# Kernel tuning notes

Measured on AMD Instinct MI355X. Metric: run time of the kernel, lower is better.

Reference implementation:

```python
import jax, jax.numpy as jnp
import numpy as np

B, S, D, U, A = 8, 2048, 1024, 1024, 4  # batch, seq, input_dim, units, n_activations


def setup_inputs() -> dict:
    key = jax.random.key(0)
    ks = jax.random.split(key, 6)
    scale_w = (6.0 / (D + U)) ** 0.5  # glorot_uniform
    scale_wf = (6.0 / (U + A)) ** 0.5
    scale_wa = (6.0 / (D + A)) ** 0.5
    return {
        "x": jax.random.normal(ks[0], (B, S, D), dtype=jnp.float32),
        "w": jax.random.uniform(ks[1], (D, U), jnp.float32, -scale_w, scale_w),
        "b": jnp.zeros((U,), jnp.float32),
        "wf": jax.random.uniform(ks[2], (U, A), jnp.float32, -scale_wf, scale_wf),
        "bf": jnp.zeros((U, A), jnp.float32),
        "w_att": jax.random.uniform(ks[3], (D, A), jnp.float32, -scale_wa, scale_wa),
        "b_att": jnp.zeros((A,), jnp.float32),
    }


def reference(x, w, b, wf, bf, w_att, b_att):
    # weighted_sum: [B,S,U]
    ws = jnp.einsum('bsd,du->bsu', x, w) + b
    # broadcast per-activation affine: [B,S,U,A]
    wa = ws[..., None] * wf + bf
    acts = [
        jax.nn.relu(wa[..., 0]),
        jax.nn.sigmoid(wa[..., 1]),
        jnp.tanh(wa[..., 2]),
        jax.nn.gelu(wa[..., 3], approximate=False),  # tf.nn.gelu default is exact
    ]
    result_activations = jnp.stack(acts, axis=-1)  # [B,S,U,A]
    # attention over activations: [B,S,A]
    attn = jax.nn.softmax(jnp.einsum('bsd,da->bsa', x, w_att) + b_att, axis=-1)
    # weighted reduce over activation axis -> [B,S,U]
    out = jnp.einsum('bsua,bsa->bsu', result_activations, attn)
    return out
```

## Files before the change

### kernel.cpp

```cpp
#include <hip/hip_runtime.h>
#include <hip/hip_bf16.h>
#include <cstdint>

#define B_ 8
#define S_ 2048
#define D_ 1024
#define U_ 1024
#define M_ (B_ * S_)

typedef __bf16 bf16x8 __attribute__((ext_vector_type(8)));
typedef float  f32x4  __attribute__((ext_vector_type(4)));

__device__ __forceinline__ uint16_t f2bf(float f) {
  uint32_t u = __builtin_bit_cast(uint32_t, f);
  u += 0x7fffu + ((u >> 16) & 1u);
  return (uint16_t)(u >> 16);
}

__device__ __forceinline__ void async_copy16(const void* g, void* l) {
  typedef const __attribute__((address_space(1))) uint8_t* gp_t;
  typedef __attribute__((address_space(3))) uint8_t* lp_t;
  __builtin_amdgcn_global_load_lds((gp_t)(uintptr_t)g,
                                   (lp_t)(uint32_t)(uintptr_t)l, 16, 0, 0);
}

__global__ __launch_bounds__(256) void k_conv_w(const float* __restrict__ w,
                                                uint16_t* __restrict__ wt) {
  __shared__ float tile[32][33];
  const int t = threadIdx.x;
  const int tx = t & 31, ty = t >> 5;
  const int c0 = blockIdx.x * 32;
  const int r0 = blockIdx.y * 32;
#pragma unroll
  for (int i = 0; i < 4; i++) {
    int r = ty + i * 8;
    tile[r][tx] = w[(size_t)(r0 + r) * U_ + c0 + tx];
  }
  __syncthreads();
#pragma unroll
  for (int i = 0; i < 4; i++) {
    int r = ty + i * 8;
    wt[(size_t)(c0 + r) * D_ + r0 + tx] = f2bf(tile[tx][r]);
  }
}

__global__ __launch_bounds__(256) void k_attn_convx(
    const float* __restrict__ x, const float* __restrict__ w_att,
    const float* __restrict__ b_att, uint16_t* __restrict__ x_bf,
    float* __restrict__ attn) {
  const int row = blockIdx.x;
  const int t = threadIdx.x;
  const float4 xv = reinterpret_cast<const float4*>(x + (size_t)row * D_)[t];
  float xe0 = xv.x, xe1 = xv.y, xe2 = xv.z, xe3 = xv.w;

  const float4* wa4 = reinterpret_cast<const float4*>(w_att);
  float p0 = 0.f, p1 = 0.f, p2 = 0.f, p3 = 0.f;
  float xs[4] = {xe0, xe1, xe2, xe3};
#pragma unroll
  for (int e = 0; e < 4; e++) {
    float4 wv = wa4[t * 4 + e];
    p0 = fmaf(xs[e], wv.x, p0);
    p1 = fmaf(xs[e], wv.y, p1);
    p2 = fmaf(xs[e], wv.z, p2);
    p3 = fmaf(xs[e], wv.w, p3);
  }

  ushort4 hb;
  hb.x = f2bf(xe0); hb.y = f2bf(xe1); hb.z = f2bf(xe2); hb.w = f2bf(xe3);
  reinterpret_cast<ushort4*>(x_bf + (size_t)row * D_)[t] = hb;

#pragma unroll
  for (int off = 32; off > 0; off >>= 1) {
    p0 += __shfl_down(p0, off);
    p1 += __shfl_down(p1, off);
    p2 += __shfl_down(p2, off);
    p3 += __shfl_down(p3, off);
  }
  __shared__ float red[4][4];
  const int lane = t & 63, wid = t >> 6;
  if (lane == 0) { red[wid][0] = p0; red[wid][1] = p1; red[wid][2] = p2; red[wid][3] = p3; }
  __syncthreads();
  if (t == 0) {
    float l0 = red[0][0] + red[1][0] + red[2][0] + red[3][0] + b_att[0];
    float l1 = red[0][1] + red[1][1] + red[2][1] + red[3][1] + b_att[1];
    float l2 = red[0][2] + red[1][2] + red[2][2] + red[3][2] + b_att[2];
    float l3 = red[0][3] + red[1][3] + red[2][3] + red[3][3] + b_att[3];
    float mx = fmaxf(fmaxf(l0, l1), fmaxf(l2, l3));
    float e0 = __expf(l0 - mx), e1 = __expf(l1 - mx);
    float e2 = __expf(l2 - mx), e3 = __expf(l3 - mx);
    float inv = 1.f / (e0 + e1 + e2 + e3);
    reinterpret_cast<float4*>(attn)[row] = make_float4(e0 * inv, e1 * inv, e2 * inv, e3 * inv);
  }
}

#define BM 128
#define BN 128
#define BK 64

__global__ __launch_bounds__(256) void k_gemm_ep(
    const uint16_t* __restrict__ xbf, const uint16_t* __restrict__ wt,
    const float* __restrict__ bias, const float* __restrict__ wf,
    const float* __restrict__ bfb, const float* __restrict__ attn,
    float* __restrict__ out) {
  __shared__ uint16_t As[BM * BK];
  __shared__ uint16_t Bs[BN * BK];

  const int t = threadIdx.x;
  const int wave = t >> 6, lane = t & 63;
  const int l16 = lane & 15, quad = lane >> 4;
  const int wm = wave >> 1, wn = wave & 1;
  const int m0 = blockIdx.y * BM;
  const int n0 = blockIdx.x * BN;

  const uint16_t* aBase = xbf + (size_t)m0 * D_;
  const uint16_t* bBase = wt + (size_t)n0 * D_;

  f32x4 acc[4][4] = {};

  for (int k0 = 0; k0 < D_; k0 += BK) {
#pragma unroll
    for (int it = 0; it < 4; it++) {
      int c = t + it * 256;
      int r = c >> 3;
      int cs = c & 7;
      int gc = cs ^ (r & 7);
      async_copy16(aBase + (size_t)r * D_ + k0 + gc * 8, (uint8_t*)As + c * 16);
      async_copy16(bBase + (size_t)r * D_ + k0 + gc * 8, (uint8_t*)Bs + c * 16);
    }
    __syncthreads();

#pragma unroll
    for (int ks = 0; ks < 2; ks++) {
      const int kcb = ks * 4;
      bf16x8 af[4], bfr[4];
#pragma unroll
      for (int i = 0; i < 4; i++) {
        int r = wm * 64 + i * 16 + l16;
        int cs = (kcb + quad) ^ (r & 7);
        af[i] = *reinterpret_cast<const bf16x8*>(&As[r * BK + cs * 8]);
      }
#pragma unroll
      for (int j = 0; j < 4; j++) {
        int n = wn * 64 + j * 16 + l16;
        int cs = (kcb + quad) ^ (n & 7);
        bfr[j] = *reinterpret_cast<const bf16x8*>(&Bs[n * BK + cs * 8]);
      }
#pragma unroll
      for (int i = 0; i < 4; i++)
#pragma unroll
        for (int j = 0; j < 4; j++)
          acc[i][j] = __builtin_amdgcn_mfma_f32_16x16x32_bf16(af[i], bfr[j], acc[i][j], 0, 0, 0);
    }
    __syncthreads();
  }

  float bu[4];
  float4 wf4[4], bf4[4];
#pragma unroll
  for (int j = 0; j < 4; j++) {
    int u = n0 + wn * 64 + j * 16 + l16;
    bu[j] = bias[u];
    wf4[j] = reinterpret_cast<const float4*>(wf)[u];
    bf4[j] = reinterpret_cast<const float4*>(bfb)[u];
  }
#pragma unroll
  for (int i = 0; i < 4; i++) {
#pragma unroll
    for (int r = 0; r < 4; r++) {
      int mg = m0 + wm * 64 + i * 16 + quad * 4 + r;
      float4 at = reinterpret_cast<const float4*>(attn)[mg];
      float* orow = out + (size_t)mg * U_;
#pragma unroll
      for (int j = 0; j < 4; j++) {
        int u = n0 + wn * 64 + j * 16 + l16;
        float wsv = acc[i][j][r] + bu[j];
        float wa0 = fmaf(wsv, wf4[j].x, bf4[j].x);
        float wa1 = fmaf(wsv, wf4[j].y, bf4[j].y);
        float wa2 = fmaf(wsv, wf4[j].z, bf4[j].z);
        float wa3 = fmaf(wsv, wf4[j].w, bf4[j].w);
        float a_relu = fmaxf(wa0, 0.f);
        float a_sig = 1.f / (1.f + __expf(-wa1));
        float ax = fabsf(wa2);
        float et = __expf(-2.f * ax);
        float a_tanh = copysignf((1.f - et) / (1.f + et), wa2);
        float a_gelu = 0.5f * wa3 * (1.f + erff(wa3 * 0.70710678118654752f));
        orow[u] = at.x * a_relu + at.y * a_sig + at.z * a_tanh + at.w * a_gelu;
      }
    }
  }
}

extern "C" void kernel_launch(void* const* d_in, const int* in_sizes, int n_in,
                              void* d_out, int out_size, void* d_ws, size_t ws_size,
                              hipStream_t stream) {
  const float* x     = (const float*)d_in[0];
  const float* w     = (const float*)d_in[1];
  const float* b     = (const float*)d_in[2];
  const float* wf    = (const float*)d_in[3];
  const float* bfb   = (const float*)d_in[4];
  const float* w_att = (const float*)d_in[5];
  const float* b_att = (const float*)d_in[6];
  float* out = (float*)d_out;

  char* ws = (char*)d_ws;
  uint16_t* x_bf = (uint16_t*)ws;
  uint16_t* w_t  = (uint16_t*)(ws + ((size_t)32 << 20));
  float*    attn = (float*)(ws + ((size_t)34 << 20));

  k_conv_w<<<dim3(U_ / 32, D_ / 32), 256, 0, stream>>>(w, w_t);
  k_attn_convx<<<dim3(M_), 256, 0, stream>>>(x, w_att, b_att, x_bf, attn);
  k_gemm_ep<<<dim3(U_ / BN, M_ / BM), 256, 0, stream>>>(x_bf, w_t, b, wf, bfb, attn, out);
}
```

Measured before the change: 197.6 us.

## Fuse prep kernels and use fast approximate activations in GEMM epilogue

Merges the weight-transpose and x-conversion/attention kernels into one launch, with one wave per row and xor-shuffle reduction, removing the cross-wave LDS reduction and one launch. Replaces exact sigmoid, tanh and erf-GELU in the epilogue with hardware exp2/rcp intrinsics and a tanh-form GELU approximation to cut transcendental cost. Adds an occupancy hint to the GEMM launch bounds. The GELU approximation changes numerics compared with exact erf and may affect tolerance.

```diff
diff --git a/kernel.cpp b/kernel.cpp
--- a/kernel.cpp
+++ b/kernel.cpp
@@ -24,72 +24,73 @@
                                    (lp_t)(uint32_t)(uintptr_t)l, 16, 0, 0);
 }
 
-__global__ __launch_bounds__(256) void k_conv_w(const float* __restrict__ w,
-                                                uint16_t* __restrict__ wt) {
+__global__ __launch_bounds__(256) void k_prep(
+    const float* __restrict__ x, const float* __restrict__ w_att,
+    const float* __restrict__ b_att, const float* __restrict__ w,
+    uint16_t* __restrict__ x_bf, float* __restrict__ attn,
+    uint16_t* __restrict__ wt) {
   __shared__ float tile[32][33];
-  const int t = threadIdx.x;
-  const int tx = t & 31, ty = t >> 5;
-  const int c0 = blockIdx.x * 32;
-  const int r0 = blockIdx.y * 32;
-#pragma unroll
-  for (int i = 0; i < 4; i++) {
-    int r = ty + i * 8;
-    tile[r][tx] = w[(size_t)(r0 + r) * U_ + c0 + tx];
-  }
-  __syncthreads();
-#pragma unroll
-  for (int i = 0; i < 4; i++) {
-    int r = ty + i * 8;
-    wt[(size_t)(c0 + r) * D_ + r0 + tx] = f2bf(tile[tx][r]);
-  }
-}
-
-__global__ __launch_bounds__(256) void k_attn_convx(
-    const float* __restrict__ x, const float* __restrict__ w_att,
-    const float* __restrict__ b_att, uint16_t* __restrict__ x_bf,
-    float* __restrict__ attn) {
-  const int row = blockIdx.x;
-  const int t = threadIdx.x;
-  const float4 xv = reinterpret_cast<const float4*>(x + (size_t)row * D_)[t];
-  float xe0 = xv.x, xe1 = xv.y, xe2 = xv.z, xe3 = xv.w;
-
-  const float4* wa4 = reinterpret_cast<const float4*>(w_att);
-  float p0 = 0.f, p1 = 0.f, p2 = 0.f, p3 = 0.f;
-  float xs[4] = {xe0, xe1, xe2, xe3};
-#pragma unroll
-  for (int e = 0; e < 4; e++) {
-    float4 wv = wa4[t * 4 + e];
-    p0 = fmaf(xs[e], wv.x, p0);
-    p1 = fmaf(xs[e], wv.y, p1);
-    p2 = fmaf(xs[e], wv.z, p2);
-    p3 = fmaf(xs[e], wv.w, p3);
-  }
-
-  ushort4 hb;
-  hb.x = f2bf(xe0); hb.y = f2bf(xe1); hb.z = f2bf(xe2); hb.w = f2bf(xe3);
-  reinterpret_cast<ushort4*>(x_bf + (size_t)row * D_)[t] = hb;
-
-#pragma unroll
-  for (int off = 32; off > 0; off >>= 1) {
-    p0 += __shfl_down(p0, off);
-    p1 += __shfl_down(p1, off);
-    p2 += __shfl_down(p2, off);
-    p3 += __shfl_down(p3, off);
-  }
-  __shared__ float red[4][4];
-  const int lane = t & 63, wid = t >> 6;
-  if (lane == 0) { red[wid][0] = p0; red[wid][1] = p1; red[wid][2] = p2; red[wid][3] = p3; }
-  __syncthreads();
-  if (t == 0) {
-    float l0 = red[0][0] + red[1][0] + red[2][0] + red[3][0] + b_att[0];
-    float l1 = red[0][1] + red[1][1] + red[2][1] + red[3][1] + b_att[1];
-    float l2 = red[0][2] + red[1][2] + red[2][2] + red[3][2] + b_att[2];
-    float l3 = red[0][3] + red[1][3] + red[2][3] + red[3][3] + b_att[3];
-    float mx = fmaxf(fmaxf(l0, l1), fmaxf(l2, l3));
-    float e0 = __expf(l0 - mx), e1 = __expf(l1 - mx);
-    float e2 = __expf(l2 - mx), e3 = __expf(l3 - mx);
-    float inv = 1.f / (e0 + e1 + e2 + e3);
-    reinterpret_cast<float4*>(attn)[row] = make_float4(e0 * inv, e1 * inv, e2 * inv, e3 * inv);
+  const int bid = blockIdx.x;
+  if (bid < M_ / 4) {
+    const int wave = threadIdx.x >> 6, lane = threadIdx.x & 63;
+    const int row = bid * 4 + wave;
+    const float4* xr = reinterpret_cast<const float4*>(x + (size_t)row * D_);
+    const float4* wa4 = reinterpret_cast<const float4*>(w_att);
+    float4 v[4];
+#pragma unroll
+    for (int i = 0; i < 4; i++) v[i] = xr[lane + 64 * i];
+    float4 p = {0.f, 0.f, 0.f, 0.f};
+#pragma unroll
+    for (int i = 0; i < 4; i++) {
+      const int base = 4 * (lane + 64 * i);
+      const float xe[4] = {v[i].x, v[i].y, v[i].z, v[i].w};
+#pragma unroll
+      for (int c = 0; c < 4; c++) {
+        float4 wv = wa4[base + c];
+        p.x = fmaf(xe[c], wv.x, p.x);
+        p.y = fmaf(xe[c], wv.y, p.y);
+        p.z = fmaf(xe[c], wv.z, p.z);
+        p.w = fmaf(xe[c], wv.w, p.w);
+      }
+      ushort4 hb;
+      hb.x = f2bf(v[i].x); hb.y = f2bf(v[i].y);
+      hb.z = f2bf(v[i].z); hb.w = f2bf(v[i].w);
+      reinterpret_cast<ushort4*>(x_bf + (size_t)row * D_)[lane + 64 * i] = hb;
+    }
+#pragma unroll
+    for (int off = 32; off > 0; off >>= 1) {
+      p.x += __shfl_xor(p.x, off);
+      p.y += __shfl_xor(p.y, off);
+      p.z += __shfl_xor(p.z, off);
+      p.w += __shfl_xor(p.w, off);
+    }
+    if (lane == 0) {
+      float l0 = p.x + b_att[0], l1 = p.y + b_att[1];
+      float l2 = p.z + b_att[2], l3 = p.w + b_att[3];
+      float mx = fmaxf(fmaxf(l0, l1), fmaxf(l2, l3));
+      float e0 = __expf(l0 - mx), e1 = __expf(l1 - mx);
+      float e2 = __expf(l2 - mx), e3 = __expf(l3 - mx);
+      float inv = __builtin_amdgcn_rcpf(e0 + e1 + e2 + e3);
+      reinterpret_cast<float4*>(attn)[row] =
+          make_float4(e0 * inv, e1 * inv, e2 * inv, e3 * inv);
+    }
+  } else {
+    const int wid = bid - M_ / 4;
+    const int t = threadIdx.x;
+    const int tx = t & 31, ty = t >> 5;
+    const int c0 = (wid & 31) * 32;
+    const int r0 = (wid >> 5) * 32;
+#pragma unroll
+    for (int i = 0; i < 4; i++) {
+      int r = ty + i * 8;
+      tile[r][tx] = w[(size_t)(r0 + r) * U_ + c0 + tx];
+    }
+    __syncthreads();
+#pragma unroll
+    for (int i = 0; i < 4; i++) {
+      int r = ty + i * 8;
+      wt[(size_t)(c0 + r) * D_ + r0 + tx] = f2bf(tile[tx][r]);
+    }
   }
 }
 
@@ -97,7 +98,7 @@
 #define BN 128
 #define BK 64
 
-__global__ __launch_bounds__(256) void k_gemm_ep(
+__global__ __launch_bounds__(256, 4) void k_gemm_ep(
     const uint16_t* __restrict__ xbf, const uint16_t* __restrict__ wt,
     const float* __restrict__ bias, const float* __restrict__ wf,
     const float* __restrict__ bfb, const float* __restrict__ attn,
@@ -179,11 +180,13 @@
         float wa2 = fmaf(wsv, wf4[j].z, bf4[j].z);
         float wa3 = fmaf(wsv, wf4[j].w, bf4[j].w);
         float a_relu = fmaxf(wa0, 0.f);
-        float a_sig = 1.f / (1.f + __expf(-wa1));
-        float ax = fabsf(wa2);
-        float et = __expf(-2.f * ax);
-        float a_tanh = copysignf((1.f - et) / (1.f + et), wa2);
-        float a_gelu = 0.5f * wa3 * (1.f + erff(wa3 * 0.70710678118654752f));
+        float a_sig = __builtin_amdgcn_rcpf(
+            1.f + __builtin_amdgcn_exp2f(-1.4426950409f * wa1));
+        float a_tanh = fmaf(2.f, __builtin_amdgcn_rcpf(
+            1.f + __builtin_amdgcn_exp2f(-2.8853900818f * wa2)), -1.f);
+        float y = wa3 * fmaf(0.044715f, wa3 * wa3, 1.f);
+        float a_gelu = wa3 * __builtin_amdgcn_rcpf(
+            1.f + __builtin_amdgcn_exp2f(-2.302207929f * y));
         orow[u] = at.x * a_relu + at.y * a_sig + at.z * a_tanh + at.w * a_gelu;
       }
     }
@@ -207,7 +210,6 @@
   uint16_t* w_t  = (uint16_t*)(ws + ((size_t)32 << 20));
   float*    attn = (float*)(ws + ((size_t)34 << 20));
 
-  k_conv_w<<<dim3(U_ / 32, D_ / 32), 256, 0, stream>>>(w, w_t);
-  k_attn_convx<<<dim3(M_), 256, 0, stream>>>(x, w_att, b_att, x_bf, attn);
+  k_prep<<<dim3(M_ / 4 + 1024), 256, 0, stream>>>(x, w_att, b_att, w, x_bf, attn, w_t);
   k_gemm_ep<<<dim3(U_ / BN, M_ / BM), 256, 0, stream>>>(x_bf, w_t, b, wf, bfb, attn, out);
 }
```

After: 178.8 us. 1.11x faster.
